# Kernel tuning notes

Measured on AMD Instinct MI355X. Metric: run time of the kernel, lower is better.

Reference implementation:

```python
import jax, jax.numpy as jnp
import numpy as np

N_NODES = 100000


def sage_conv(x, src, dst, Wl, bl, Wr):
    # mean aggregation of source features at target nodes
    msg_sum = jax.ops.segment_sum(x[src], dst, num_segments=N_NODES)  # [N, C]
    deg = jax.ops.segment_sum(jnp.ones_like(src, dtype=x.dtype), dst, num_segments=N_NODES)
    agg = msg_sum / jnp.maximum(deg, 1.0)[:, None]
    return agg @ Wl + bl + x @ Wr


def setup_inputs() -> dict:
    key = jax.random.key(0)
    ks = jax.random.split(key, 6)
    N, E, C_in, C_hid, C_out = N_NODES, 400000, 128, 256, 64
    x = jax.random.normal(ks[0], (N, C_in), dtype=jnp.float32)
    edge_index = jax.random.randint(ks[1], (2, E), 0, N, dtype=jnp.int64)
    s = 1.0 / np.sqrt(C_in)
    W1l = jax.random.normal(ks[2], (C_in, C_hid), dtype=jnp.float32) * s
    W1r = jax.random.normal(ks[3], (C_in, C_hid), dtype=jnp.float32) * s
    b1 = jnp.zeros((C_hid,), dtype=jnp.float32)
    s2 = 1.0 / np.sqrt(C_hid)
    W2l = jax.random.normal(ks[4], (C_hid, C_out), dtype=jnp.float32) * s2
    W2r = jax.random.normal(ks[5], (C_hid, C_out), dtype=jnp.float32) * s2
    b2 = jnp.zeros((C_out,), dtype=jnp.float32)
    return {"x": x, "edge_index": edge_index, "W1l": W1l, "b1": b1, "W1r": W1r,
            "W2l": W2l, "b2": b2, "W2r": W2r}


def reference(x, edge_index, W1l, b1, W1r, W2l, b2, W2r):
    src, dst = edge_index[0], edge_index[1]
    h = sage_conv(x, src, dst, W1l, b1, W1r)
    h = jax.nn.relu(h)  # dropout is identity in eval mode
    out = sage_conv(h, src, dst, W2l, b2, W2r)
    return out
```

## Files before the change

### kernel.cpp

```cpp
#include <hip/hip_runtime.h>
#include <cstddef>

#define N_NODES 100000
#define E_EDGES 400000
#define C_IN    128
#define C_HID   256
#define C_OUT   64

typedef __attribute__((ext_vector_type(8))) short bf16x8;
typedef __attribute__((ext_vector_type(4))) float f32x4;

__device__ __forceinline__ unsigned short f2bf(float f) {
    union { float f; unsigned u; } x; x.f = f;
    unsigned r = x.u + 0x7fffu + ((x.u >> 16) & 1u);
    return (unsigned short)(r >> 16);
}

__global__ void hist_kernel(const int* __restrict__ dst, int* __restrict__ deg, int E) {
    int e = blockIdx.x * blockDim.x + threadIdx.x;
    if (e < E) atomicAdd(&deg[dst[e]], 1);
}

__global__ __launch_bounds__(256) void scan_partial(const int* __restrict__ deg,
                                                    int* __restrict__ bsums, int n) {
    __shared__ int red[256];
    int base = blockIdx.x * 2048 + threadIdx.x * 8;
    int s = 0;
    #pragma unroll
    for (int i = 0; i < 8; ++i) { int idx = base + i; if (idx < n) s += deg[idx]; }
    red[threadIdx.x] = s; __syncthreads();
    for (int off = 128; off > 0; off >>= 1) {
        if (threadIdx.x < off) red[threadIdx.x] += red[threadIdx.x + off];
        __syncthreads();
    }
    if (threadIdx.x == 0) bsums[blockIdx.x] = red[0];
}

__global__ __launch_bounds__(64) void scan_bsums(int* __restrict__ bsums, int nb) {
    __shared__ int s[64];
    int t = threadIdx.x;
    s[t] = (t < nb) ? bsums[t] : 0; __syncthreads();
    for (int off = 1; off < 64; off <<= 1) {
        int v = (t >= off) ? s[t - off] : 0;
        __syncthreads();
        s[t] += v;
        __syncthreads();
    }
    if (t < nb) bsums[t] = (t == 0) ? 0 : s[t - 1];
}

__global__ __launch_bounds__(256) void scan_apply(const int* __restrict__ deg,
                                                  const int* __restrict__ bsums,
                                                  int* __restrict__ row_start,
                                                  int* __restrict__ cursor, int n, int E) {
    __shared__ int red[256];
    int t = threadIdx.x;
    int base = blockIdx.x * 2048 + t * 8;
    int v[8]; int s = 0;
    #pragma unroll
    for (int i = 0; i < 8; ++i) { int idx = base + i; v[i] = (idx < n) ? deg[idx] : 0; s += v[i]; }
    red[t] = s; __syncthreads();
    for (int off = 1; off < 256; off <<= 1) {
        int u = (t >= off) ? red[t - off] : 0;
        __syncthreads();
        red[t] += u;
        __syncthreads();
    }
    int run = bsums[blockIdx.x] + ((t == 0) ? 0 : red[t - 1]);
    #pragma unroll
    for (int i = 0; i < 8; ++i) {
        int idx = base + i;
        if (idx < n) { row_start[idx] = run; cursor[idx] = run; run += v[i]; }
    }
    if (blockIdx.x == 0 && t == 0) row_start[n] = E;
}

__global__ void fill_kernel(const int* __restrict__ src, const int* __restrict__ dst,
                            int* __restrict__ cursor, int* __restrict__ nbr, int E) {
    int e = blockIdx.x * blockDim.x + threadIdx.x;
    if (e < E) {
        int pos = atomicAdd(&cursor[dst[e]], 1);
        nbr[pos] = src[e];
    }
}

template<int C>
__global__ void gather_mean_kernel(const int* __restrict__ row_start,
                                   const int* __restrict__ nbr,
                                   const float* __restrict__ feat,
                                   float* __restrict__ out, int N) {
    constexpr int LPN = C / 4;
    const int gid  = blockIdx.x * blockDim.x + threadIdx.x;
    const int node = gid / LPN;
    const int lane = gid - node * LPN;
    if (node >= N) return;
    const int s = row_start[node];
    const int e = row_start[node + 1];
    float4 acc = make_float4(0.f, 0.f, 0.f, 0.f);
    const float4* f4 = reinterpret_cast<const float4*>(feat);
    for (int j = s; j < e; ++j) {
        const float4 v = f4[(size_t)nbr[j] * LPN + lane];
        acc.x += v.x; acc.y += v.y; acc.z += v.z; acc.w += v.w;
    }
    const float inv = 1.0f / (float)((e - s) > 1 ? (e - s) : 1);
    acc.x *= inv; acc.y *= inv; acc.z *= inv; acc.w *= inv;
    reinterpret_cast<float4*>(out)[(size_t)node * LPN + lane] = acc;
}

__global__ void gather_out_kernel(const int* __restrict__ row_start,
                                  const int* __restrict__ nbr,
                                  const float* __restrict__ t2,
                                  const float* __restrict__ u,
                                  const float* __restrict__ b2,
                                  float* __restrict__ out, int N) {
    const int gid  = blockIdx.x * blockDim.x + threadIdx.x;
    const int node = gid >> 4;
    const int lane = gid & 15;
    if (node >= N) return;
    const int s = row_start[node];
    const int e = row_start[node + 1];
    float4 acc = make_float4(0.f, 0.f, 0.f, 0.f);
    const float4* f4 = reinterpret_cast<const float4*>(t2);
    for (int j = s; j < e; ++j) {
        const float4 v = f4[(size_t)nbr[j] * 16 + lane];
        acc.x += v.x; acc.y += v.y; acc.z += v.z; acc.w += v.w;
    }
    const float inv = 1.0f / (float)((e - s) > 1 ? (e - s) : 1);
    const float4 uv = reinterpret_cast<const float4*>(u)[(size_t)node * 16 + lane];
    const float4 bv = reinterpret_cast<const float4*>(b2)[lane];
    float4 o;
    o.x = acc.x * inv + uv.x + bv.x;
    o.y = acc.y * inv + uv.y + bv.y;
    o.z = acc.z * inv + uv.z + bv.z;
    o.w = acc.w * inv + uv.w + bv.w;
    reinterpret_cast<float4*>(out)[(size_t)node * 16 + lane] = o;
}

__global__ void w1T_kernel(const float* __restrict__ W1l, const float* __restrict__ W1r,
                           unsigned short* __restrict__ W1T) {
    int n = blockIdx.x, k = threadIdx.x;
    float v = (k < 128) ? W1l[(size_t)k * 256 + n] : W1r[(size_t)(k - 128) * 256 + n];
    W1T[(size_t)n * 256 + k] = f2bf(v);
}
__global__ void w2T_kernel(const float* __restrict__ W2l, const float* __restrict__ W2r,
                           unsigned short* __restrict__ WT2) {
    int n = blockIdx.x, k = threadIdx.x;
    float v = (n < 64) ? W2l[(size_t)k * 64 + n] : W2r[(size_t)k * 64 + (n - 64)];
    WT2[(size_t)n * 256 + k] = f2bf(v);
}

__device__ __forceinline__ int swz(int row, int slotByte) {
    return row * 64 + (slotByte ^ (((row >> 1) & 3) << 4));
}

__global__ __launch_bounds__(256) void gemm1_mfma(
        const float* __restrict__ Agg,
        const float* __restrict__ X,
        const unsigned short* __restrict__ W1T,
        const float* __restrict__ bias,
        unsigned short* __restrict__ H,
        int M)
{
    __shared__ __align__(16) unsigned short As[64 * 32];
    __shared__ __align__(16) unsigned short Bs[256 * 32];

    const int tid  = threadIdx.x;
    const int wave = tid >> 6, lane = tid & 63;
    const int m0 = blockIdx.x * 64;

    const int a_row = tid >> 2;
    const int a_seg = tid & 3;
    int gm = m0 + a_row; if (gm >= M) gm = M - 1;

    f32x4 acc[4][4];
    #pragma unroll
    for (int m = 0; m < 4; ++m)
        #pragma unroll
        for (int n = 0; n < 4; ++n) acc[m][n] = (f32x4){0.f, 0.f, 0.f, 0.f};

    const int kb = lane >> 4;
    const int lr = lane & 15;

    for (int k0 = 0; k0 < 256; k0 += 32) {
        {
            const float* srcp = (k0 < 128)
                ? (Agg + (size_t)gm * 128 + k0 + a_seg * 8)
                : (X   + (size_t)gm * 128 + (k0 - 128) + a_seg * 8);
            const float4 v0 = *reinterpret_cast<const float4*>(srcp);
            const float4 v1 = *reinterpret_cast<const float4*>(srcp + 4);
            int4 w;
            w.x = (int)f2bf(v0.x) | ((int)f2bf(v0.y) << 16);
            w.y = (int)f2bf(v0.z) | ((int)f2bf(v0.w) << 16);
            w.z = (int)f2bf(v1.x) | ((int)f2bf(v1.y) << 16);
            w.w = (int)f2bf(v1.z) | ((int)f2bf(v1.w) << 16);
            *reinterpret_cast<int4*>((char*)As + swz(a_row, a_seg * 16)) = w;
        }
        #pragma unroll
        for (int i = 0; i < 4; ++i) {
            int c = tid + 256 * i, row = c >> 2, slot = c & 3;
            int4 v = *reinterpret_cast<const int4*>(W1T + (size_t)row * 256 + k0 + slot * 8);
            *reinterpret_cast<int4*>((char*)Bs + swz(row, slot * 16)) = v;
        }
        __syncthreads();

        bf16x8 af[4], bfr[4];
        #pragma unroll
        for (int m = 0; m < 4; ++m)
            af[m] = *reinterpret_cast<const bf16x8*>((const char*)As + swz(m * 16 + lr, kb * 16));
        #pragma unroll
        for (int n = 0; n < 4; ++n)
            bfr[n] = *reinterpret_cast<const bf16x8*>(
                (const char*)Bs + swz(wave * 64 + n * 16 + lr, kb * 16));
        #pragma unroll
        for (int m = 0; m < 4; ++m)
            #pragma unroll
            for (int n = 0; n < 4; ++n)
                acc[m][n] = __builtin_amdgcn_mfma_f32_16x16x32_bf16(af[m], bfr[n], acc[m][n], 0, 0, 0);
        __syncthreads();
    }

    #pragma unroll
    for (int m = 0; m < 4; ++m) {
        const int gr_base = m0 + m * 16 + (lane >> 4) * 4;
        #pragma unroll
        for (int n = 0; n < 4; ++n) {
            const int gc = wave * 64 + n * 16 + (lane & 15);
            const float b = bias[gc];
            #pragma unroll
            for (int r = 0; r < 4; ++r) {
                const int gr = gr_base + r;
                if (gr < M) {
                    float v = acc[m][n][r] + b;
                    H[(size_t)gr * 256 + gc] = f2bf(fmaxf(v, 0.0f));
                }
            }
        }
    }
}

__global__ __launch_bounds__(256) void gemm2_dual(
        const unsigned short* __restrict__ H,
        const unsigned short* __restrict__ WT2,
        float* __restrict__ t2,
        float* __restrict__ u,
        int M)
{
    __shared__ __align__(16) unsigned short As[64 * 32];
    __shared__ __align__(16) unsigned short Bs[128 * 32];

    const int tid  = threadIdx.x;
    const int wave = tid >> 6, lane = tid & 63;
    const int m0 = blockIdx.x * 64;

    const int a_row = tid >> 2;
    const int a_seg = tid & 3;
    int gm = m0 + a_row; if (gm >= M) gm = M - 1;

    f32x4 acc[4][2];
    #pragma unroll
    for (int m = 0; m < 4; ++m)
        #pragma unroll
        for (int n = 0; n < 2; ++n) acc[m][n] = (f32x4){0.f, 0.f, 0.f, 0.f};

    const int kb = lane >> 4;
    const int lr = lane & 15;

    for (int k0 = 0; k0 < 256; k0 += 32) {
        {
            int4 v = *reinterpret_cast<const int4*>(H + (size_t)gm * 256 + k0 + a_seg * 8);
            *reinterpret_cast<int4*>((char*)As + swz(a_row, a_seg * 16)) = v;
        }
        #pragma unroll
        for (int i = 0; i < 2; ++i) {
            int c = tid + 256 * i, row = c >> 2, slot = c & 3;
            int4 v = *reinterpret_cast<const int4*>(WT2 + (size_t)row * 256 + k0 + slot * 8);
            *reinterpret_cast<int4*>((char*)Bs + swz(row, slot * 16)) = v;
        }
        __syncthreads();

        bf16x8 af[4], bfr[2];
        #pragma unroll
        for (int m = 0; m < 4; ++m)
            af[m] = *reinterpret_cast<const bf16x8*>((const char*)As + swz(m * 16 + lr, kb * 16));
        #pragma unroll
        for (int n = 0; n < 2; ++n)
            bfr[n] = *reinterpret_cast<const bf16x8*>(
                (const char*)Bs + swz(wave * 32 + n * 16 + lr, kb * 16));
        #pragma unroll
        for (int m = 0; m < 4; ++m)
            #pragma unroll
            for (int n = 0; n < 2; ++n)
                acc[m][n] = __builtin_amdgcn_mfma_f32_16x16x32_bf16(af[m], bfr[n], acc[m][n], 0, 0, 0);
        __syncthreads();
    }

    #pragma unroll
    for (int m = 0; m < 4; ++m) {
        const int gr_base = m0 + m * 16 + (lane >> 4) * 4;
        #pragma unroll
        for (int n = 0; n < 2; ++n) {
            const int gc = wave * 32 + n * 16 + (lane & 15);
            float* dstp = (gc < 64) ? (t2 + gc) : (u + (gc - 64));
            #pragma unroll
            for (int r = 0; r < 4; ++r) {
                const int gr = gr_base + r;
                if (gr < M) dstp[(size_t)gr * 64] = acc[m][n][r];
            }
        }
    }
}

extern "C" void kernel_launch(void* const* d_in, const int* in_sizes, int n_in,
                              void* d_out, int out_size, void* d_ws, size_t ws_size,
                              hipStream_t stream) {
    const float* x    = (const float*)d_in[0];
    const int*   eidx = (const int*)d_in[1];
    const float* W1l  = (const float*)d_in[2];
    const float* b1   = (const float*)d_in[3];
    const float* W1r  = (const float*)d_in[4];
    const float* W2l  = (const float*)d_in[5];
    const float* b2   = (const float*)d_in[6];
    const float* W2r  = (const float*)d_in[7];
    float* out = (float*)d_out;

    const int* src = eidx;
    const int* dst = eidx + E_EDGES;
    const int N = N_NODES, E = E_EDGES;
    const int NSCAN = (N + 2047) / 2048;

    int*   deg_i     = (int*)d_ws;
    int*   row_start = deg_i + N;
    int*   cursor    = row_start + (N + 1);
    int*   nbr       = cursor + N;
    int*   bsums     = nbr + E;
    char*  fb        = (char*)(((size_t)(bsums + 64) + 15) & ~(size_t)15);
    unsigned short* W1T = (unsigned short*)fb;
    unsigned short* WT2 = W1T + 256 * 256;
    float* agg1      = (float*)(WT2 + 128 * 256);
    unsigned short* h = (unsigned short*)(agg1 + (size_t)N * C_IN);
    float* t2        = agg1;
    float* u         = t2 + (size_t)N * C_OUT;

    hipMemsetAsync(deg_i, 0, (size_t)N * sizeof(int), stream);
    hist_kernel<<<(E + 255) / 256, 256, 0, stream>>>(dst, deg_i, E);
    scan_partial<<<NSCAN, 256, 0, stream>>>(deg_i, bsums, N);
    scan_bsums<<<1, 64, 0, stream>>>(bsums, NSCAN);
    scan_apply<<<NSCAN, 256, 0, stream>>>(deg_i, bsums, row_start, cursor, N, E);
    fill_kernel<<<(E + 255) / 256, 256, 0, stream>>>(src, dst, cursor, nbr, E);

    w1T_kernel<<<256, 256, 0, stream>>>(W1l, W1r, W1T);
    w2T_kernel<<<128, 256, 0, stream>>>(W2l, W2r, WT2);

    gather_mean_kernel<C_IN><<<((size_t)N * (C_IN / 4) + 255) / 256, 256, 0, stream>>>(
        row_start, nbr, x, agg1, N);
    gemm1_mfma<<<(N + 63) / 64, 256, 0, stream>>>(agg1, x, W1T, b1, h, N);

    gemm2_dual<<<(N + 63) / 64, 256, 0, stream>>>(h, WT2, t2, u, N);
    gather_out_kernel<<<((size_t)N * 16 + 255) / 256, 256, 0, stream>>>(
        row_start, nbr, t2, u, b2, out, N);
}
```

Before: 304.5 us.

## Store gathered features and intermediates in bf16 to halve gather traffic

Converts x to bf16 once, then runs the layer-1 mean aggregation over bf16 rows, accumulating in fp32, and writes the aggregate as bf16. gemm1 now loads bf16 directly with no in-kernel conversion. gemm2 writes the t2 half as bf16 so the output gather also reads half-size rows. The aim is to roughly halve the random-gather memory traffic in both aggregation kernels, at the cost of an extra conversion pass over x and some loss of precision in the gathered values.

```diff
diff --git a/kernel.cpp b/kernel.cpp
--- a/kernel.cpp
+++ b/kernel.cpp
@@ -14,6 +14,12 @@
     union { float f; unsigned u; } x; x.f = f;
     unsigned r = x.u + 0x7fffu + ((x.u >> 16) & 1u);
     return (unsigned short)(r >> 16);
+}
+__device__ __forceinline__ float bflo(int u) {
+    union { int i; float f; } x; x.i = u << 16; return x.f;
+}
+__device__ __forceinline__ float bfhi(int u) {
+    union { int i; float f; } x; x.i = u & 0xffff0000; return x.f;
 }
 
 __global__ void hist_kernel(const int* __restrict__ dst, int* __restrict__ deg, int E) {
@@ -84,56 +90,85 @@
     }
 }
 
-template<int C>
-__global__ void gather_mean_kernel(const int* __restrict__ row_start,
-                                   const int* __restrict__ nbr,
-                                   const float* __restrict__ feat,
-                                   float* __restrict__ out, int N) {
-    constexpr int LPN = C / 4;
-    const int gid  = blockIdx.x * blockDim.x + threadIdx.x;
-    const int node = gid / LPN;
-    const int lane = gid - node * LPN;
-    if (node >= N) return;
-    const int s = row_start[node];
-    const int e = row_start[node + 1];
-    float4 acc = make_float4(0.f, 0.f, 0.f, 0.f);
-    const float4* f4 = reinterpret_cast<const float4*>(feat);
-    for (int j = s; j < e; ++j) {
-        const float4 v = f4[(size_t)nbr[j] * LPN + lane];
-        acc.x += v.x; acc.y += v.y; acc.z += v.z; acc.w += v.w;
-    }
-    const float inv = 1.0f / (float)((e - s) > 1 ? (e - s) : 1);
-    acc.x *= inv; acc.y *= inv; acc.z *= inv; acc.w *= inv;
-    reinterpret_cast<float4*>(out)[(size_t)node * LPN + lane] = acc;
-}
-
-__global__ void gather_out_kernel(const int* __restrict__ row_start,
-                                  const int* __restrict__ nbr,
-                                  const float* __restrict__ t2,
-                                  const float* __restrict__ u,
-                                  const float* __restrict__ b2,
-                                  float* __restrict__ out, int N) {
+__global__ void cvt_x_kernel(const float* __restrict__ in,
+                             unsigned short* __restrict__ out, int n8) {
+    int i = blockIdx.x * blockDim.x + threadIdx.x;
+    if (i >= n8) return;
+    const float4* p = reinterpret_cast<const float4*>(in) + (size_t)i * 2;
+    const float4 a = p[0], b = p[1];
+    int4 w;
+    w.x = (int)f2bf(a.x) | ((int)f2bf(a.y) << 16);
+    w.y = (int)f2bf(a.z) | ((int)f2bf(a.w) << 16);
+    w.z = (int)f2bf(b.x) | ((int)f2bf(b.y) << 16);
+    w.w = (int)f2bf(b.z) | ((int)f2bf(b.w) << 16);
+    reinterpret_cast<int4*>(out)[i] = w;
+}
+
+__global__ void gather_mean_bf16(const int* __restrict__ row_start,
+                                 const int* __restrict__ nbr,
+                                 const unsigned short* __restrict__ xbf,
+                                 unsigned short* __restrict__ aggbf, int N) {
     const int gid  = blockIdx.x * blockDim.x + threadIdx.x;
     const int node = gid >> 4;
     const int lane = gid & 15;
     if (node >= N) return;
     const int s = row_start[node];
     const int e = row_start[node + 1];
-    float4 acc = make_float4(0.f, 0.f, 0.f, 0.f);
-    const float4* f4 = reinterpret_cast<const float4*>(t2);
+    float acc[8] = {0.f, 0.f, 0.f, 0.f, 0.f, 0.f, 0.f, 0.f};
+    const int4* f = reinterpret_cast<const int4*>(xbf);
     for (int j = s; j < e; ++j) {
-        const float4 v = f4[(size_t)nbr[j] * 16 + lane];
-        acc.x += v.x; acc.y += v.y; acc.z += v.z; acc.w += v.w;
+        const int4 v = f[(size_t)nbr[j] * 16 + lane];
+        acc[0] += bflo(v.x); acc[1] += bfhi(v.x);
+        acc[2] += bflo(v.y); acc[3] += bfhi(v.y);
+        acc[4] += bflo(v.z); acc[5] += bfhi(v.z);
+        acc[6] += bflo(v.w); acc[7] += bfhi(v.w);
     }
     const float inv = 1.0f / (float)((e - s) > 1 ? (e - s) : 1);
-    const float4 uv = reinterpret_cast<const float4*>(u)[(size_t)node * 16 + lane];
-    const float4 bv = reinterpret_cast<const float4*>(b2)[lane];
-    float4 o;
-    o.x = acc.x * inv + uv.x + bv.x;
-    o.y = acc.y * inv + uv.y + bv.y;
-    o.z = acc.z * inv + uv.z + bv.z;
-    o.w = acc.w * inv + uv.w + bv.w;
-    reinterpret_cast<float4*>(out)[(size_t)node * 16 + lane] = o;
+    int4 w;
+    w.x = (int)f2bf(acc[0] * inv) | ((int)f2bf(acc[1] * inv) << 16);
+    w.y = (int)f2bf(acc[2] * inv) | ((int)f2bf(acc[3] * inv) << 16);
+    w.z = (int)f2bf(acc[4] * inv) | ((int)f2bf(acc[5] * inv) << 16);
+    w.w = (int)f2bf(acc[6] * inv) | ((int)f2bf(acc[7] * inv) << 16);
+    reinterpret_cast<int4*>(aggbf)[(size_t)node * 16 + lane] = w;
+}
+
+__global__ void gather_out_kernel(const int* __restrict__ row_start,
+                                  const int* __restrict__ nbr,
+                                  const unsigned short* __restrict__ t2bf,
+                                  const float* __restrict__ u,
+                                  const float* __restrict__ b2,
+                                  float* __restrict__ out, int N) {
+    const int gid  = blockIdx.x * blockDim.x + threadIdx.x;
+    const int node = gid >> 3;
+    const int lane = gid & 7;
+    if (node >= N) return;
+    const int s = row_start[node];
+    const int e = row_start[node + 1];
+    float acc[8] = {0.f, 0.f, 0.f, 0.f, 0.f, 0.f, 0.f, 0.f};
+    const int4* f = reinterpret_cast<const int4*>(t2bf);
+    for (int j = s; j < e; ++j) {
+        const int4 v = f[(size_t)nbr[j] * 8 + lane];
+        acc[0] += bflo(v.x); acc[1] += bfhi(v.x);
+        acc[2] += bflo(v.y); acc[3] += bfhi(v.y);
+        acc[4] += bflo(v.z); acc[5] += bfhi(v.z);
+        acc[6] += bflo(v.w); acc[7] += bfhi(v.w);
+    }
+    const float inv = 1.0f / (float)((e - s) > 1 ? (e - s) : 1);
+    const float4* up = reinterpret_cast<const float4*>(u) + (size_t)node * 16 + lane * 2;
+    const float4 u0 = up[0], u1 = up[1];
+    const float4 b0 = reinterpret_cast<const float4*>(b2)[lane * 2];
+    const float4 b1 = reinterpret_cast<const float4*>(b2)[lane * 2 + 1];
+    float4 o0, o1;
+    o0.x = acc[0] * inv + u0.x + b0.x;
+    o0.y = acc[1] * inv + u0.y + b0.y;
+    o0.z = acc[2] * inv + u0.z + b0.z;
+    o0.w = acc[3] * inv + u0.w + b0.w;
+    o1.x = acc[4] * inv + u1.x + b1.x;
+    o1.y = acc[5] * inv + u1.y + b1.y;
+    o1.z = acc[6] * inv + u1.z + b1.z;
+    o1.w = acc[7] * inv + u1.w + b1.w;
+    float4* op = reinterpret_cast<float4*>(out) + (size_t)node * 16 + lane * 2;
+    op[0] = o0; op[1] = o1;
 }
 
 __global__ void w1T_kernel(const float* __restrict__ W1l, const float* __restrict__ W1r,
@@ -154,8 +189,8 @@
 }
 
 __global__ __launch_bounds__(256) void gemm1_mfma(
-        const float* __restrict__ Agg,
-        const float* __restrict__ X,
+        const unsigned short* __restrict__ AggBf,
+        const unsigned short* __restrict__ XBf,
         const unsigned short* __restrict__ W1T,
         const float* __restrict__ bias,
         unsigned short* __restrict__ H,
@@ -183,17 +218,11 @@
 
     for (int k0 = 0; k0 < 256; k0 += 32) {
         {
-            const float* srcp = (k0 < 128)
-                ? (Agg + (size_t)gm * 128 + k0 + a_seg * 8)
-                : (X   + (size_t)gm * 128 + (k0 - 128) + a_seg * 8);
-            const float4 v0 = *reinterpret_cast<const float4*>(srcp);
-            const float4 v1 = *reinterpret_cast<const float4*>(srcp + 4);
-            int4 w;
-            w.x = (int)f2bf(v0.x) | ((int)f2bf(v0.y) << 16);
-            w.y = (int)f2bf(v0.z) | ((int)f2bf(v0.w) << 16);
-            w.z = (int)f2bf(v1.x) | ((int)f2bf(v1.y) << 16);
-            w.w = (int)f2bf(v1.z) | ((int)f2bf(v1.w) << 16);
-            *reinterpret_cast<int4*>((char*)As + swz(a_row, a_seg * 16)) = w;
+            const unsigned short* srcp = (k0 < 128)
+                ? (AggBf + (size_t)gm * 128 + k0 + a_seg * 8)
+                : (XBf   + (size_t)gm * 128 + (k0 - 128) + a_seg * 8);
+            int4 v = *reinterpret_cast<const int4*>(srcp);
+            *reinterpret_cast<int4*>((char*)As + swz(a_row, a_seg * 16)) = v;
         }
         #pragma unroll
         for (int i = 0; i < 4; ++i) {
@@ -241,7 +270,7 @@
 __global__ __launch_bounds__(256) void gemm2_dual(
         const unsigned short* __restrict__ H,
         const unsigned short* __restrict__ WT2,
-        float* __restrict__ t2,
+        unsigned short* __restrict__ t2bf,
         float* __restrict__ u,
         int M)
 {
@@ -300,11 +329,13 @@
         #pragma unroll
         for (int n = 0; n < 2; ++n) {
             const int gc = wave * 32 + n * 16 + (lane & 15);
-            float* dstp = (gc < 64) ? (t2 + gc) : (u + (gc - 64));
             #pragma unroll
             for (int r = 0; r < 4; ++r) {
                 const int gr = gr_base + r;
-                if (gr < M) dstp[(size_t)gr * 64] = acc[m][n][r];
+                if (gr < M) {
+                    if (gc < 64) t2bf[(size_t)gr * 64 + gc] = f2bf(acc[m][n][r]);
+                    else         u[(size_t)gr * 64 + (gc - 64)] = acc[m][n][r];
+                }
             }
         }
     }
@@ -334,12 +365,17 @@
     int*   nbr       = cursor + N;
     int*   bsums     = nbr + E;
     char*  fb        = (char*)(((size_t)(bsums + 64) + 15) & ~(size_t)15);
-    unsigned short* W1T = (unsigned short*)fb;
-    unsigned short* WT2 = W1T + 256 * 256;
-    float* agg1      = (float*)(WT2 + 128 * 256);
-    unsigned short* h = (unsigned short*)(agg1 + (size_t)N * C_IN);
-    float* t2        = agg1;
-    float* u         = t2 + (size_t)N * C_OUT;
+    unsigned short* W1T    = (unsigned short*)fb;
+    unsigned short* WT2    = W1T + 256 * 256;
+    unsigned short* x_bf   = WT2 + 128 * 256;
+    unsigned short* agg_bf = x_bf + (size_t)N * C_IN;
+    unsigned short* h      = agg_bf + (size_t)N * C_IN;
+    unsigned short* t2bf   = h + (size_t)N * C_HID;
+    float* u = (float*)(((size_t)(t2bf + (size_t)N * C_OUT) + 15) & ~(size_t)15);
+
+    cvt_x_kernel<<<(N * C_IN / 8 + 255) / 256, 256, 0, stream>>>(x, x_bf, N * C_IN / 8);
+    w1T_kernel<<<256, 256, 0, stream>>>(W1l, W1r, W1T);
+    w2T_kernel<<<128, 256, 0, stream>>>(W2l, W2r, WT2);
 
     hipMemsetAsync(deg_i, 0, (size_t)N * sizeof(int), stream);
     hist_kernel<<<(E + 255) / 256, 256, 0, stream>>>(dst, deg_i, E);
@@ -348,14 +384,11 @@
     scan_apply<<<NSCAN, 256, 0, stream>>>(deg_i, bsums, row_start, cursor, N, E);
     fill_kernel<<<(E + 255) / 256, 256, 0, stream>>>(src, dst, cursor, nbr, E);
 
-    w1T_kernel<<<256, 256, 0, stream>>>(W1l, W1r, W1T);
-    w2T_kernel<<<128, 256, 0, stream>>>(W2l, W2r, WT2);
-
-    gather_mean_kernel<C_IN><<<((size_t)N * (C_IN / 4) + 255) / 256, 256, 0, stream>>>(
-        row_start, nbr, x, agg1, N);
-    gemm1_mfma<<<(N + 63) / 64, 256, 0, stream>>>(agg1, x, W1T, b1, h, N);
-
-    gemm2_dual<<<(N + 63) / 64, 256, 0, stream>>>(h, WT2, t2, u, N);
-    gather_out_kernel<<<((size_t)N * 16 + 255) / 256, 256, 0, stream>>>(
-        row_start, nbr, t2, u, b2, out, N);
-}
+    gather_mean_bf16<<<((size_t)N * 16 + 255) / 256, 256, 0, stream>>>(
+        row_start, nbr, x_bf, agg_bf, N);
+    gemm1_mfma<<<(N + 63) / 64, 256, 0, stream>>>(agg_bf, x_bf, W1T, b1, h, N);
+
+    gemm2_dual<<<(N + 63) / 64, 256, 0, stream>>>(h, WT2, t2bf, u, N);
+    gather_out_kernel<<<((size_t)N * 8 + 255) / 256, 256, 0, stream>>>(
+        row_start, nbr, t2bf, u, b2, out, N);
+}
```

After: 289.9 us. -4.8%, faster.
